# Kernel tuning notes

Hardware: AMD Instinct MI355X
Metric: run time of the kernel (lower is better)

Reference implementation:

```python
import jax, jax.numpy as jnp
import numpy as np

B, S, C, MID = 32, 8192, 256, 128

def setup_inputs() -> dict:
    key = jax.random.key(0)
    k_x, k_w1, k_b1, k_w2, k_b2 = jax.random.split(key, 5)
    bound1 = 1.0 / np.sqrt(C)
    bound2 = 1.0 / np.sqrt(MID)
    return {
        "x": jax.random.normal(k_x, (B, S, C), dtype=jnp.float32),
        "W1": jax.random.uniform(k_w1, (C, MID), jnp.float32, -bound1, bound1),
        "b1": jax.random.uniform(k_b1, (MID,), jnp.float32, -bound1, bound1),
        "w2": jax.random.uniform(k_w2, (MID,), jnp.float32, -bound2, bound2),
        "b2": jax.random.uniform(k_b2, (), jnp.float32, -bound2, bound2),
    }

def reference(x, W1, b1, w2, b2):
    # scores: (B, S) — dropout is identity in eval mode
    h = jnp.tanh(jnp.einsum("bsc,cm->bsm", x, W1) + b1)       # (B, S, MID)
    scores = jnp.einsum("bsm,m->bs", h, w2) + b2              # (B, S)
    attn = jax.nn.softmax(scores, axis=-1)                    # softmax over seq
    out = jnp.einsum("bsc,bs->bc", x, attn)                   # weighted sum over seq
    return out
```

## Files before the change

### kernel.cpp

```cpp
#include <hip/hip_runtime.h>
#include <hip/hip_bf16.h>


typedef __attribute__((ext_vector_type(8))) short short8;
typedef __attribute__((ext_vector_type(4))) float f32x4;
typedef unsigned short u16;

constexpr int Bb = 32;
constexpr int Ss = 8192;
constexpr int Cc = 256;
constexpr int MIDm = 128;
constexpr int BM = 128;
constexpr int BK = 32;
constexpr int NCH = Cc / BK;
constexpr int NBLK = Bb * Ss / BM;
constexpr int BPB = Ss / BM;

__device__ __forceinline__ u16 f2bf(float f) {
  return __builtin_bit_cast(u16, __float2bfloat16(f));
}

__global__ __launch_bounds__(256) void wprep_kernel(
    const float* __restrict__ W1, u16* __restrict__ FB)
{
  const int t    = blockIdx.x * 256 + threadIdx.x;
  const int lane = t & 63;
  const int nt   = (t >> 6) & 3;
  const int kcc  = (t >> 8) & 7;
  const int wc   = (t >> 11) & 1;
  const int n    = wc * 64 + nt * 16 + (lane & 15);
  const int k0   = kcc * 32 + (lane >> 4) * 8;
  union { u16 v[8]; short8 s; } u;
  #pragma unroll
  for (int e = 0; e < 8; ++e) u.v[e] = f2bf(W1[(size_t)(k0 + e) * MIDm + n]);
  *(short8*)(FB + (size_t)t * 8) = u.s;
}

__global__ __launch_bounds__(256, 4) void fused_kernel(
    const float* __restrict__ x, const u16* __restrict__ FB,
    const float* __restrict__ b1, const float* __restrict__ w2,
    float* __restrict__ oPart, float* __restrict__ mPart, float* __restrict__ lPart)
{
  __shared__ __align__(16) char sX[2][BM * BK * 4];
  __shared__ float sScore[2][BM];
  __shared__ float sP[BM];
  __shared__ float sMB, sLB;
  __shared__ __align__(16) float sO[4][Cc];

  const int tid  = threadIdx.x;
  const int lane = tid & 63;
  const int w    = tid >> 6;
  const int wr   = w >> 1;
  const int wc   = w & 1;
  const int q    = lane >> 4;
  const int ln   = lane & 15;
  const int row0 = blockIdx.x * BM;

  f32x4 acc[4][4];
  #pragma unroll
  for (int nt = 0; nt < 4; ++nt) {
    float bj = b1[64 * wc + 16 * nt + ln];
    #pragma unroll
    for (int mt = 0; mt < 4; ++mt) {
      acc[mt][nt][0] = bj; acc[mt][nt][1] = bj; acc[mt][nt][2] = bj; acc[mt][nt][3] = bj;
    }
  }

  const u16* fb = FB + ((size_t)wc * 2048 + lane) * 8;
  #define LDFRAG(kcc, nt) (*(const short8*)(fb + ((size_t)(kcc) * 256 + (nt) * 64) * 8))

  #define STAGE(buf, kc)                                                              \
    {                                                                                 \
      _Pragma("unroll")                                                               \
      for (int r = 0; r < 4; ++r) {                                                   \
        int L   = r * 4096 + tid * 16;                                                \
        int row = L >> 7;                                                             \
        int cb  = (L & 127) ^ ((row & 7) << 4);                                       \
        const char* src = (const char*)x                                              \
            + ((size_t)(row0 + row) * Cc + (size_t)(kc) * BK) * 4 + cb;               \
        __builtin_amdgcn_global_load_lds(                                             \
            (const __attribute__((address_space(1))) void*)src,                       \
            (__attribute__((address_space(3))) void*)(&sX[buf][0] + L),               \
            16, 0, 0);                                                                \
      }                                                                               \
    }

  short8 bfr[2][4];

  STAGE(0, 0);
  #pragma unroll
  for (int nt = 0; nt < 4; ++nt) bfr[0][nt] = LDFRAG(0, nt);
  __syncthreads();

  #pragma unroll
  for (int kc = 0; kc < NCH; ++kc) {
    const int cur = kc & 1;
    if (kc < NCH - 1) {
      STAGE(1 - cur, kc + 1);
      #pragma unroll
      for (int nt = 0; nt < 4; ++nt) bfr[1 - cur][nt] = LDFRAG(kc + 1, nt);
    }

    #pragma unroll
    for (int mt = 0; mt < 4; ++mt) {
      const int row = 64 * wr + 16 * mt + ln;
      const int s   = (row & 7) << 4;
      const char* base = &sX[cur][0] + row * 128;
      float4 lo = *(const float4*)(base + ((q * 32) ^ s));
      float4 hi = *(const float4*)(base + ((q * 32 + 16) ^ s));
      union { u16 v[8]; short8 s8; } t8;
      t8.v[0] = f2bf(lo.x); t8.v[1] = f2bf(lo.y); t8.v[2] = f2bf(lo.z); t8.v[3] = f2bf(lo.w);
      t8.v[4] = f2bf(hi.x); t8.v[5] = f2bf(hi.y); t8.v[6] = f2bf(hi.z); t8.v[7] = f2bf(hi.w);
      #pragma unroll
      for (int nt = 0; nt < 4; ++nt)
        acc[mt][nt] = __builtin_amdgcn_mfma_f32_16x16x32_bf16(
            t8.s8, bfr[cur][nt], acc[mt][nt], 0, 0, 0);
    }
    if (kc < NCH - 1) __syncthreads();
  }

  float w2v[4];
  #pragma unroll
  for (int nt = 0; nt < 4; ++nt) w2v[nt] = w2[64 * wc + 16 * nt + ln];

  float p[4][4];
  #pragma unroll
  for (int mt = 0; mt < 4; ++mt)
    #pragma unroll
    for (int r = 0; r < 4; ++r) p[mt][r] = 0.f;

  #pragma unroll
  for (int mt = 0; mt < 4; ++mt)
    #pragma unroll
    for (int nt = 0; nt < 4; ++nt)
      #pragma unroll
      for (int r = 0; r < 4; ++r)
        p[mt][r] += (1.0f - 2.0f / (__expf(2.0f * acc[mt][nt][r]) + 1.0f)) * w2v[nt];

  #pragma unroll
  for (int off = 1; off < 16; off <<= 1)
    #pragma unroll
    for (int mt = 0; mt < 4; ++mt)
      #pragma unroll
      for (int r = 0; r < 4; ++r)
        p[mt][r] += __shfl_xor(p[mt][r], off);

  if (ln == 0) {
    #pragma unroll
    for (int mt = 0; mt < 4; ++mt)
      #pragma unroll
      for (int r = 0; r < 4; ++r)
        sScore[wc][64 * wr + 16 * mt + 4 * q + r] = p[mt][r];
  }
  __syncthreads();

  if (tid < BM) sP[tid] = sScore[0][tid] + sScore[1][tid];
  __syncthreads();
  if (w == 0) {
    float a = sP[lane], b = sP[lane + 64];
    float m = fmaxf(a, b);
    #pragma unroll
    for (int off = 1; off < 64; off <<= 1) m = fmaxf(m, __shfl_xor(m, off));
    float e0 = __expf(a - m), e1 = __expf(b - m);
    sP[lane] = e0; sP[lane + 64] = e1;
    float s = e0 + e1;
    #pragma unroll
    for (int off = 1; off < 64; off <<= 1) s += __shfl_xor(s, off);
    if (lane == 0) { sMB = m; sLB = s; }
  }
  __syncthreads();

  const int c4 = tid & 63;
  const int rg = tid >> 6;
  const float* xo = x + (size_t)(row0 + rg * 32) * Cc + c4 * 4;
  float4 o = make_float4(0.f, 0.f, 0.f, 0.f);
  #pragma unroll 8
  for (int r = 0; r < 32; ++r) {
    float pw = sP[rg * 32 + r];
    float4 xv = *(const float4*)(xo + (size_t)r * Cc);
    o.x = fmaf(pw, xv.x, o.x);
    o.y = fmaf(pw, xv.y, o.y);
    o.z = fmaf(pw, xv.z, o.z);
    o.w = fmaf(pw, xv.w, o.w);
  }
  *(float4*)&sO[rg][c4 * 4] = o;
  __syncthreads();

  float oc = sO[0][tid] + sO[1][tid] + sO[2][tid] + sO[3][tid];
  oPart[(size_t)blockIdx.x * Cc + tid] = oc;
  if (tid == 0) { mPart[blockIdx.x] = sMB; lPart[blockIdx.x] = sLB; }
}

__global__ __launch_bounds__(256) void combine_kernel(
    const float* __restrict__ oPart, const float* __restrict__ mPart,
    const float* __restrict__ lPart, float* __restrict__ out)
{
  const int b = blockIdx.x;
  const int t = threadIdx.x;
  float M = -3.4e38f;
  for (int k = 0; k < BPB; ++k) M = fmaxf(M, mPart[b * BPB + k]);
  float num = 0.f, den = 0.f;
  for (int k = 0; k < BPB; ++k) {
    float wgt = __expf(mPart[b * BPB + k] - M);
    den += wgt * lPart[b * BPB + k];
    num = fmaf(wgt, oPart[(size_t)(b * BPB + k) * Cc + t], num);
  }
  out[b * Cc + t] = num / den;
}

extern "C" void kernel_launch(void* const* d_in, const int* in_sizes, int n_in,
                              void* d_out, int out_size, void* d_ws, size_t ws_size,
                              hipStream_t stream)
{
  const float* x  = (const float*)d_in[0];
  const float* W1 = (const float*)d_in[1];
  const float* b1 = (const float*)d_in[2];
  const float* w2 = (const float*)d_in[3];
  float* out = (float*)d_out;

  u16*   FB    = (u16*)d_ws;
  float* oPart = (float*)((char*)d_ws + 65536);
  float* mPart = (float*)((char*)d_ws + 65536 + 2097152);
  float* lPart = (float*)((char*)d_ws + 65536 + 2097152 + 8192);

  wprep_kernel<<<16, 256, 0, stream>>>(W1, FB);
  fused_kernel<<<NBLK, 256, 0, stream>>>(x, FB, b1, w2, oPart, mPart, lPart);
  combine_kernel<<<Bb, Cc, 0, stream>>>(oPart, mPart, lPart, out);
}
```

Measured before the change: 107.3 us.

## Stage W1 fragments through LDS with async loads and explicit vmcnt pipelining

Preconverted bf16 W1 fragments are now copied into double-buffered LDS with global_load_lds alongside the x tiles, so each wave no longer holds them in registers. Hand-placed s_waitcnt vmcnt and raw s_barrier calls replace __syncthreads, letting the next chunk's loads stay in flight during MFMA work. Shared memory is merged into one 48KB buffer reused for the epilogue, and launch bounds drop from 4 to 3 blocks per SM. The cost is more LDS traffic and lower occupancy, and correctness relies on the manual waitcnt count matching the six loads issued per stage.

```diff
diff --git a/kernel.cpp b/kernel.cpp
--- a/kernel.cpp
+++ b/kernel.cpp
@@ -36,16 +36,14 @@
   *(short8*)(FB + (size_t)t * 8) = u.s;
 }
 
-__global__ __launch_bounds__(256, 4) void fused_kernel(
+__global__ __launch_bounds__(256, 3) void fused_kernel(
     const float* __restrict__ x, const u16* __restrict__ FB,
     const float* __restrict__ b1, const float* __restrict__ w2,
     float* __restrict__ oPart, float* __restrict__ mPart, float* __restrict__ lPart)
 {
-  __shared__ __align__(16) char sX[2][BM * BK * 4];
-  __shared__ float sScore[2][BM];
-  __shared__ float sP[BM];
-  __shared__ float sMB, sLB;
-  __shared__ __align__(16) float sO[4][Cc];
+  __shared__ __align__(16) char smem[49152];
+  #define SXA(buf) (smem + (buf) * 16384)
+  #define SBB(buf) (smem + 32768 + (buf) * 8192)
 
   const int tid  = threadIdx.x;
   const int lane = tid & 63;
@@ -66,10 +64,7 @@
     }
   }
 
-  const u16* fb = FB + ((size_t)wc * 2048 + lane) * 8;
-  #define LDFRAG(kcc, nt) (*(const short8*)(fb + ((size_t)(kcc) * 256 + (nt) * 64) * 8))
-
-  #define STAGE(buf, kc)                                                              \
+  #define STAGE_ALL(buf, kc)                                                          \
     {                                                                                 \
       _Pragma("unroll")                                                               \
       for (int r = 0; r < 4; ++r) {                                                   \
@@ -80,32 +75,45 @@
             + ((size_t)(row0 + row) * Cc + (size_t)(kc) * BK) * 4 + cb;               \
         __builtin_amdgcn_global_load_lds(                                             \
             (const __attribute__((address_space(1))) void*)src,                       \
-            (__attribute__((address_space(3))) void*)(&sX[buf][0] + L),               \
+            (__attribute__((address_space(3))) void*)(SXA(buf) + L),                  \
+            16, 0, 0);                                                                \
+      }                                                                               \
+      _Pragma("unroll")                                                               \
+      for (int r = 0; r < 2; ++r) {                                                   \
+        const char* srcb = (const char*)FB                                            \
+            + ((size_t)r * 2048 + (size_t)(kc) * 256) * 16 + (size_t)tid * 16;        \
+        __builtin_amdgcn_global_load_lds(                                             \
+            (const __attribute__((address_space(1))) void*)srcb,                      \
+            (__attribute__((address_space(3))) void*)(SBB(buf) + r * 4096 + tid * 16),\
             16, 0, 0);                                                                \
       }                                                                               \
     }
 
-  short8 bfr[2][4];
-
-  STAGE(0, 0);
-  #pragma unroll
-  for (int nt = 0; nt < 4; ++nt) bfr[0][nt] = LDFRAG(0, nt);
-  __syncthreads();
+  STAGE_ALL(0, 0);
 
   #pragma unroll
   for (int kc = 0; kc < NCH; ++kc) {
     const int cur = kc & 1;
-    if (kc < NCH - 1) {
-      STAGE(1 - cur, kc + 1);
-      #pragma unroll
-      for (int nt = 0; nt < 4; ++nt) bfr[1 - cur][nt] = LDFRAG(kc + 1, nt);
-    }
+    if (kc < NCH - 1) STAGE_ALL(1 - cur, kc + 1);
+
+    __builtin_amdgcn_sched_barrier(0);
+    if (kc < NCH - 1) asm volatile("s_waitcnt vmcnt(6)");
+    else              asm volatile("s_waitcnt vmcnt(0)");
+    __builtin_amdgcn_sched_barrier(0);
+    __builtin_amdgcn_s_barrier();
+    __builtin_amdgcn_sched_barrier(0);
+
+    const char* bb = SBB(cur) + wc * 4096 + lane * 16;
+    short8 bfrag[4];
+    #pragma unroll
+    for (int nt = 0; nt < 4; ++nt)
+      bfrag[nt] = *(const short8*)(bb + nt * 1024);
 
     #pragma unroll
     for (int mt = 0; mt < 4; ++mt) {
       const int row = 64 * wr + 16 * mt + ln;
       const int s   = (row & 7) << 4;
-      const char* base = &sX[cur][0] + row * 128;
+      const char* base = SXA(cur) + row * 128;
       float4 lo = *(const float4*)(base + ((q * 32) ^ s));
       float4 hi = *(const float4*)(base + ((q * 32 + 16) ^ s));
       union { u16 v[8]; short8 s8; } t8;
@@ -114,10 +122,17 @@
       #pragma unroll
       for (int nt = 0; nt < 4; ++nt)
         acc[mt][nt] = __builtin_amdgcn_mfma_f32_16x16x32_bf16(
-            t8.s8, bfr[cur][nt], acc[mt][nt], 0, 0, 0);
+            t8.s8, bfrag[nt], acc[mt][nt], 0, 0, 0);
     }
-    if (kc < NCH - 1) __syncthreads();
-  }
+
+    __builtin_amdgcn_sched_barrier(0);
+    __builtin_amdgcn_s_barrier();
+  }
+
+  float* sScore = (float*)smem;
+  float* sP     = (float*)(smem + 1024);
+  float* sO     = (float*)(smem + 2048);
+  float* sML    = (float*)(smem + 6144);
 
   float w2v[4];
   #pragma unroll
@@ -150,11 +165,11 @@
     for (int mt = 0; mt < 4; ++mt)
       #pragma unroll
       for (int r = 0; r < 4; ++r)
-        sScore[wc][64 * wr + 16 * mt + 4 * q + r] = p[mt][r];
-  }
-  __syncthreads();
-
-  if (tid < BM) sP[tid] = sScore[0][tid] + sScore[1][tid];
+        sScore[wc * BM + 64 * wr + 16 * mt + 4 * q + r] = p[mt][r];
+  }
+  __syncthreads();
+
+  if (tid < BM) sP[tid] = sScore[tid] + sScore[BM + tid];
   __syncthreads();
   if (w == 0) {
     float a = sP[lane], b = sP[lane + 64];
@@ -166,7 +181,7 @@
     float s = e0 + e1;
     #pragma unroll
     for (int off = 1; off < 64; off <<= 1) s += __shfl_xor(s, off);
-    if (lane == 0) { sMB = m; sLB = s; }
+    if (lane == 0) { sML[0] = m; sML[1] = s; }
   }
   __syncthreads();
 
@@ -183,12 +198,12 @@
     o.z = fmaf(pw, xv.z, o.z);
     o.w = fmaf(pw, xv.w, o.w);
   }
-  *(float4*)&sO[rg][c4 * 4] = o;
-  __syncthreads();
-
-  float oc = sO[0][tid] + sO[1][tid] + sO[2][tid] + sO[3][tid];
+  *(float4*)&sO[rg * Cc + c4 * 4] = o;
+  __syncthreads();
+
+  float oc = sO[tid] + sO[Cc + tid] + sO[2 * Cc + tid] + sO[3 * Cc + tid];
   oPart[(size_t)blockIdx.x * Cc + tid] = oc;
-  if (tid == 0) { mPart[blockIdx.x] = sMB; lPart[blockIdx.x] = sLB; }
+  if (tid == 0) { mPart[blockIdx.x] = sML[0]; lPart[blockIdx.x] = sML[1]; }
 }
 
 __global__ __launch_bounds__(256) void combine_kernel(
```

Result: faster. 95.36 us (-11.1%).
